# Kernel tuning notes

Measured on AMD Instinct MI355X. Metric: run time of the kernel, lower is better.

The kernel has to match this reference:

```python
import jax, jax.numpy as jnp
import numpy as np
import math

HEADS = 16
HIDDEN = 2048
D_K = HIDDEN // HEADS
BATCH = 2
SEQ = 2048
ROPE_THETA = 10000.0


def make_freqs_cis(seq_len, d_k, theta=ROPE_THETA):
    # Llama rotary frequencies; returned as (seq, d_k//2, 2) = (cos, sin)
    inv_freq = 1.0 / (theta ** (np.arange(0, d_k, 2, dtype=np.float32) / d_k))
    t = np.arange(seq_len, dtype=np.float32)
    ang = np.outer(t, inv_freq)  # (seq, d_k//2)
    return jnp.asarray(np.stack([np.cos(ang), np.sin(ang)], axis=-1))


def setup_inputs() -> dict:
    key = jax.random.key(0)
    ks = jax.random.split(key, 5)
    scale = 1.0 / math.sqrt(HIDDEN)
    return {
        "x": jax.random.normal(ks[0], (BATCH, SEQ, HIDDEN), dtype=jnp.float32),
        "freqs_cis": make_freqs_cis(SEQ, D_K),
        "wq": jax.random.normal(ks[1], (HIDDEN, HIDDEN), dtype=jnp.float32) * scale,
        "wk": jax.random.normal(ks[2], (HIDDEN, HIDDEN), dtype=jnp.float32) * scale,
        "wv": jax.random.normal(ks[3], (HIDDEN, HIDDEN), dtype=jnp.float32) * scale,
        "wo": jax.random.normal(ks[4], (HIDDEN, HIDDEN), dtype=jnp.float32) * scale,
    }


def _apply_rope(t, cos, sin):
    # t: (B, S, h, d_k); cos/sin: (1, S, 1, d_k//2)
    B, S, h, dk = t.shape
    tp = t.reshape(B, S, h, dk // 2, 2)
    t0, t1 = tp[..., 0], tp[..., 1]
    r0 = t0 * cos - t1 * sin
    r1 = t0 * sin + t1 * cos
    return jnp.stack([r0, r1], axis=-1).reshape(B, S, h, dk)


def reference(x, freqs_cis, wq, wk, wv, wo):
    B, S, H = x.shape
    h, dk = HEADS, H // HEADS
    # nn.Linear(bias=False): y = x @ W.T
    q = (x @ wq.T).reshape(B, S, h, dk)
    k = (x @ wk.T).reshape(B, S, h, dk)
    v = (x @ wv.T).reshape(B, S, h, dk)
    cos = freqs_cis[None, :, None, :, 0]
    sin = freqs_cis[None, :, None, :, 1]
    q = _apply_rope(q, cos, sin)
    k = _apply_rope(k, cos, sin)
    # (B, h, S, dk)
    q = q.transpose(0, 2, 1, 3)
    k = k.transpose(0, 2, 1, 3)
    v = v.transpose(0, 2, 1, 3)
    scores = jnp.einsum("bhqd,bhkd->bhqk", q, k) / math.sqrt(dk)
    causal = jnp.tril(jnp.ones((S, S), dtype=bool))
    scores = jnp.where(causal[None, None], scores, -jnp.inf)
    attn = jax.nn.softmax(scores, axis=-1)
    out = jnp.einsum("bhqk,bhkd->bhqd", attn, v)
    out = out.transpose(0, 2, 1, 3).reshape(B, S, H)
    return out @ wo.T
```

## Files before the change

kernel.cpp:

```cpp
#include <hip/hip_runtime.h>

#define SEQ 2048
#define HID 2048
#define NH 16
#define DK 128
#define NTOK 4096

typedef __bf16 bf16x8 __attribute__((ext_vector_type(8)));
typedef float f32x4 __attribute__((ext_vector_type(4)));
typedef unsigned int u32x4 __attribute__((ext_vector_type(4)));

__device__ __forceinline__ unsigned short f2bf(float f) {
  unsigned int u = __builtin_bit_cast(unsigned int, f);
  u += 0x7fffu + ((u >> 16) & 1u);
  return (unsigned short)(u >> 16);
}
__device__ __forceinline__ float bf2f(unsigned int lo16) {
  return __builtin_bit_cast(float, lo16 << 16);
}

__device__ __forceinline__ void async_cp16(const void* g, void* l) {
  __builtin_amdgcn_global_load_lds(
      (__attribute__((address_space(1))) void*)const_cast<void*>(g),
      (__attribute__((address_space(3))) void*)l, 16, 0, 0);
}

__global__ void convert_all_kernel(const float* __restrict__ x,
                                   const float* __restrict__ wq,
                                   const float* __restrict__ wk,
                                   const float* __restrict__ wv,
                                   const float* __restrict__ wo,
                                   const float* __restrict__ fc,
                                   unsigned short* __restrict__ xb,
                                   unsigned short* __restrict__ wqb,
                                   unsigned short* __restrict__ wkb,
                                   unsigned short* __restrict__ wvb,
                                   unsigned short* __restrict__ wob,
                                   unsigned int* __restrict__ fcb) {
  const int bid = blockIdx.x;
  if (bid >= 24576) {
    const int idx = (bid - 24576) * 256 + threadIdx.x;
    const int s = idx >> 6, d = idx & 63;
    const float2 cs = *(const float2*)(fc + s * 128 + 2 * d);
    fcb[idx] = (unsigned int)f2bf(cs.x) | ((unsigned int)f2bf(cs.y) << 16);
    return;
  }
  const float* src;
  unsigned short* dst;
  int base;
  if (bid < 8192) {
    src = x; dst = xb; base = bid;
  } else {
    const int t = (bid - 8192) >> 12;
    base = (bid - 8192) & 4095;
    src = (t == 0) ? wq : (t == 1) ? wk : (t == 2) ? wv : wo;
    dst = (t == 0) ? wqb : (t == 1) ? wkb : (t == 2) ? wvb : wob;
  }
  const int i = base * 256 + threadIdx.x;
  float4 v = ((const float4*)src)[i];
  ushort4 o;
  o.x = f2bf(v.x); o.y = f2bf(v.y); o.z = f2bf(v.z); o.w = f2bf(v.w);
  ((ushort4*)dst)[i] = o;
}

template<bool F32OUT>
__global__ __launch_bounds__(256, 2)
void gemm_bt_kernel(const unsigned short* __restrict__ A,
                    const unsigned short* __restrict__ B0,
                    const unsigned short* __restrict__ B1,
                    const unsigned short* __restrict__ B2,
                    unsigned short* __restrict__ O0,
                    unsigned short* __restrict__ O1,
                    unsigned short* __restrict__ O2,
                    float* __restrict__ Of,
                    const unsigned int* __restrict__ fcb) {
  __shared__ alignas(16) unsigned short As[128 * 64];
  __shared__ alignas(16) unsigned short Bs[128 * 64];

  const int bx = blockIdx.x, by = blockIdx.y;
  const unsigned short* B;
  unsigned short* Ob = nullptr;
  int sel = 0, col0;
  if (F32OUT) {
    B = B0;
    col0 = bx * 128;
  } else {
    sel = bx >> 4;
    B = (sel == 0) ? B0 : (sel == 1) ? B1 : B2;
    Ob = (sel == 0) ? O0 : (sel == 1) ? O1 : O2;
    col0 = (bx & 15) * 128;
  }
  const int row0 = by * 128;

  const int tid = threadIdx.x;
  const int wave = tid >> 6, lane = tid & 63;
  const int quad = lane >> 4, r = lane & 15;
  const int wm = wave >> 1, wn = wave & 1;
  const int jbase = wave * 256 + lane;

  f32x4 acc[4][4] = {};

  for (int k0 = 0; k0 < HID; k0 += 64) {
    for (int t = 0; t < 4; ++t) {
      const int j = jbase + t * 64;
      const int m = j >> 3;
      const int gc = (j & 7) ^ (m & 7);
      async_cp16(A + (size_t)(row0 + m) * HID + k0 + gc * 8, As + j * 8);
      async_cp16(B + (size_t)(col0 + m) * HID + k0 + gc * 8, Bs + j * 8);
    }
    __syncthreads();
    for (int kk = 0; kk < 2; ++kk) {
      bf16x8 af[4], bfr[4];
      for (int mt = 0; mt < 4; ++mt) {
        const int m = wm * 64 + mt * 16 + r;
        const int slot = (kk * 4 + quad) ^ (m & 7);
        af[mt] = __builtin_bit_cast(bf16x8, *(const u32x4*)(As + m * 64 + slot * 8));
      }
      for (int nt = 0; nt < 4; ++nt) {
        const int n = wn * 64 + nt * 16 + r;
        const int slot = (kk * 4 + quad) ^ (n & 7);
        bfr[nt] = __builtin_bit_cast(bf16x8, *(const u32x4*)(Bs + n * 64 + slot * 8));
      }
      for (int mt = 0; mt < 4; ++mt)
        for (int nt = 0; nt < 4; ++nt)
          acc[mt][nt] = __builtin_amdgcn_mfma_f32_16x16x32_bf16(
              af[mt], bfr[nt], acc[mt][nt], 0, 0, 0);
    }
    __syncthreads();
  }

  if (!F32OUT && sel == 2) {
    for (int mt = 0; mt < 4; ++mt) {
      const int row = row0 + wm * 64 + mt * 16 + quad * 4;
      const int b = row >> 11, s = row & (SEQ - 1);
      for (int nt = 0; nt < 4; ++nt) {
        const int col = col0 + wn * 64 + nt * 16 + r;
        ushort4 pk;
        pk.x = f2bf(acc[mt][nt][0]);
        pk.y = f2bf(acc[mt][nt][1]);
        pk.z = f2bf(acc[mt][nt][2]);
        pk.w = f2bf(acc[mt][nt][3]);
        *(ushort4*)(Ob + ((size_t)(b * HID + col)) * SEQ + s) = pk;
      }
    }
    return;
  }

  if (!F32OUT) {
    const float qs = (sel == 0) ? 0.12751743f : 1.0f;
    for (int mt = 0; mt < 4; ++mt) {
      const int row = row0 + wm * 64 + mt * 16 + quad * 4;
      for (int nt = 0; nt < 4; ++nt) {
        const int col = col0 + wn * 64 + nt * 16 + r;
        const int d = (wn * 64 + nt * 16 + r) >> 1;
        for (int v = 0; v < 4; ++v) {
          const int s = (row + v) & (SEQ - 1);
          const unsigned int u = fcb[s * 64 + d];
          const float c = bf2f(u & 0xffffu), sn = bf2f(u >> 16);
          const float val = acc[mt][nt][v];
          const float par = __shfl_xor(val, 1, 64);
          const float res = (r & 1) ? (par * sn + val * c)
                                    : (val * c - par * sn);
          Ob[(size_t)(row + v) * HID + col] = f2bf(res * qs);
        }
      }
    }
    return;
  }

  for (int mt = 0; mt < 4; ++mt) {
    const int row = row0 + wm * 64 + mt * 16 + quad * 4;
    for (int nt = 0; nt < 4; ++nt) {
      const int col = col0 + wn * 64 + nt * 16 + r;
      for (int v = 0; v < 4; ++v)
        Of[(size_t)(row + v) * HID + col] = acc[mt][nt][v];
    }
  }
}

__global__ __launch_bounds__(256, 2)
void flash_attn_kernel(const unsigned short* __restrict__ Qb,
                       const unsigned short* __restrict__ Kb,
                       const unsigned short* __restrict__ VtG,
                       unsigned short* __restrict__ Ob) {
  __shared__ alignas(16) unsigned short KsA[64 * 128];
  __shared__ alignas(16) unsigned short KsB[64 * 128];
  __shared__ alignas(16) unsigned short VsA[128 * 64];
  __shared__ alignas(16) unsigned short VsB[128 * 64];
  __shared__ alignas(16) unsigned short Ps[4][16 * 64];

  const int bx = blockIdx.x, bh = blockIdx.y;
  const int tid = threadIdx.x, wave = tid >> 6, lane = tid & 63;
  const int quad = lane >> 4, r = lane & 15;
  const int tokbase = (bh >> 4) * SEQ;
  const int h = bh & 15;

  const u32x4 onesv = {0x3F803F80u, 0x3F803F80u, 0x3F803F80u, 0x3F803F80u};

  auto stage = [&](int kt, unsigned short* Ks, unsigned short* Vs) {
    for (int t = 0; t < 4; ++t) {
      const int j = t * 256 + tid;
      const int n = j >> 4, slot = j & 15;
      const int gc = (slot & 8) | ((slot & 7) ^ (n & 7));
      async_cp16(Kb + (size_t)(tokbase + kt * 64 + n) * HID + h * DK + gc * 8,
                 Ks + j * 8);
    }
    for (int t = 0; t < 4; ++t) {
      const int j = t * 256 + tid;
      const int d = j >> 3, slot = j & 7;
      const int gc = slot ^ (d & 7);
      async_cp16(VtG + ((size_t)(bh * DK + d)) * SEQ + kt * 64 + gc * 8,
                 Vs + j * 8);
    }
  };

  for (int phase = 0; phase < 2; ++phase) {
    const int qt = phase ? (31 - bx) : bx;
    const int q0 = qt * 64;

    u32x4 qf[4];
    {
      const unsigned short* qrow =
          Qb + (size_t)(tokbase + q0 + wave * 16 + r) * HID + h * DK;
      for (int kk = 0; kk < 4; ++kk)
        qf[kk] = *(const u32x4*)(qrow + kk * 32 + quad * 8);
    }

    f32x4 o[8] = {};
    float m_i[4], l_i[4];
    for (int v = 0; v < 4; ++v) { m_i[v] = -__builtin_inff(); l_i[v] = 0.f; }

    auto body = [&](const unsigned short* Ks, const unsigned short* Vs, int kt) {
      f32x4 s[4];
      for (int nt = 0; nt < 4; ++nt) {
        f32x4 a = {};
        const int n = nt * 16 + r;
        for (int kk = 0; kk < 4; ++kk) {
          const int c = kk * 4 + quad;
          const int slot = (c & 8) | ((c & 7) ^ (r & 7));
          u32x4 bkf = *(const u32x4*)(Ks + n * 128 + slot * 8);
          a = __builtin_amdgcn_mfma_f32_16x16x32_bf16(
              __builtin_bit_cast(bf16x8, qf[kk]),
              __builtin_bit_cast(bf16x8, bkf), a, 0, 0, 0);
        }
        s[nt] = a;
      }

      if (kt == qt) {
        const int qrow_g = q0 + wave * 16 + quad * 4;
        for (int nt = 0; nt < 4; ++nt) {
          const int col = kt * 64 + nt * 16 + r;
          for (int v = 0; v < 4; ++v)
            if (col > qrow_g + v) s[nt][v] = -__builtin_inff();
        }
      }

      float mx[4];
      for (int v = 0; v < 4; ++v)
        mx[v] = fmaxf(fmaxf(s[0][v], s[1][v]), fmaxf(s[2][v], s[3][v]));
      for (int off = 1; off < 16; off <<= 1)
        for (int v = 0; v < 4; ++v)
          mx[v] = fmaxf(mx[v], __shfl_xor(mx[v], off, 64));

      float alpha[4];
      for (int v = 0; v < 4; ++v) {
        const float mnew = fmaxf(m_i[v], mx[v]);
        alpha[v] = exp2f(m_i[v] - mnew);
        m_i[v] = mnew;
      }

      unsigned short* ps = &Ps[wave][0];
      for (int nt = 0; nt < 4; ++nt) {
        const int chunk = nt * 2 + (r >> 3);
        for (int v = 0; v < 4; ++v) {
          const float p = exp2f(s[nt][v] - m_i[v]);
          const int row = quad * 4 + v;
          const int slot = chunk ^ (row & 7);
          ps[row * 64 + slot * 8 + (r & 7)] = f2bf(p);
        }
      }
      for (int dt = 0; dt < 8; ++dt)
        for (int v = 0; v < 4; ++v)
          o[dt][v] *= alpha[v];
      __asm__ volatile("" ::: "memory");

      f32x4 rsacc = {};
      for (int kk2 = 0; kk2 < 2; ++kk2) {
        const int c = kk2 * 4 + quad;
        const int aslot = c ^ (r & 7);
        u32x4 pa = *(const u32x4*)(ps + r * 64 + aslot * 8);
        rsacc = __builtin_amdgcn_mfma_f32_16x16x32_bf16(
            __builtin_bit_cast(bf16x8, pa),
            __builtin_bit_cast(bf16x8, onesv), rsacc, 0, 0, 0);
        for (int dt = 0; dt < 8; ++dt) {
          const int d = dt * 16 + r;
          const int bslot = c ^ (d & 7);
          u32x4 bv = *(const u32x4*)(Vs + d * 64 + bslot * 8);
          o[dt] = __builtin_amdgcn_mfma_f32_16x16x32_bf16(
              __builtin_bit_cast(bf16x8, pa),
              __builtin_bit_cast(bf16x8, bv), o[dt], 0, 0, 0);
        }
      }
      for (int v = 0; v < 4; ++v)
        l_i[v] = l_i[v] * alpha[v] + rsacc[v];
    };

    stage(0, KsA, VsA);
    int kt = 0;
    while (true) {
      __syncthreads();
      if (kt + 1 <= qt) stage(kt + 1, KsB, VsB);
      body(KsA, VsA, kt);
      if (++kt > qt) break;
      __syncthreads();
      if (kt + 1 <= qt) stage(kt + 1, KsA, VsA);
      body(KsB, VsB, kt);
      if (++kt > qt) break;
    }

    float li[4];
    for (int v = 0; v < 4; ++v) li[v] = 1.f / l_i[v];
    for (int dt = 0; dt < 8; ++dt)
      for (int v = 0; v < 4; ++v) {
        const size_t row = (size_t)tokbase + q0 + wave * 16 + quad * 4 + v;
        Ob[row * HID + h * DK + dt * 16 + r] = f2bf(o[dt][v] * li[v]);
      }
    __syncthreads();
  }
}

extern "C" void kernel_launch(void* const* d_in, const int* in_sizes, int n_in,
                              void* d_out, int out_size, void* d_ws, size_t ws_size,
                              hipStream_t stream) {
  const float* x  = (const float*)d_in[0];
  const float* fc = (const float*)d_in[1];
  const float* wq = (const float*)d_in[2];
  const float* wk = (const float*)d_in[3];
  const float* wv = (const float*)d_in[4];
  const float* wo = (const float*)d_in[5];
  float* out = (float*)d_out;

  unsigned short* xb  = (unsigned short*)d_ws;
  unsigned short* wqb = xb  + (size_t)NTOK * HID;
  unsigned short* wkb = wqb + (size_t)HID * HID;
  unsigned short* wvb = wkb + (size_t)HID * HID;
  unsigned short* wob = wvb + (size_t)HID * HID;
  unsigned short* qb  = wob + (size_t)HID * HID;
  unsigned short* kb  = qb  + (size_t)NTOK * HID;
  unsigned short* vtb = kb  + (size_t)NTOK * HID;
  unsigned short* ab  = vtb + (size_t)NTOK * HID;
  unsigned int*   fcb = (unsigned int*)(ab + (size_t)NTOK * HID);

  convert_all_kernel<<<24576 + 512, 256, 0, stream>>>(
      x, wq, wk, wv, wo, fc, xb, wqb, wkb, wvb, wob, fcb);

  gemm_bt_kernel<false><<<dim3(48, 32), 256, 0, stream>>>(
      xb, wqb, wkb, wvb, qb, kb, vtb, nullptr, fcb);

  flash_attn_kernel<<<dim3(16, 32), 256, 0, stream>>>(qb, kb, vtb, ab);

  gemm_bt_kernel<true><<<dim3(16, 32), 256, 0, stream>>>(
      ab, wob, nullptr, nullptr, nullptr, nullptr, nullptr, out, fcb);
}
```

Before: 375.6 us.

## Rewrite flash attention with 32x32 MFMA, transposed scores and split-K waves

Reworks the attention inner loop to use 32x32x16 bf16 MFMA with a transposed S = K·Q^T layout, so each lane holds one query's scores in registers. Two waves split each 64-key tile and their partial outputs are merged through LDS at the end. The LDS round trip for P and the ones-vector MFMA for row sums are replaced by in-register bf16 packing with permlane32 swaps and a direct sum. It also adds a lazy rescale that skips the output correction while the running max grows by at most 8, plus s_setprio hints around the MFMA blocks. The cost is an extra LDS merge with barriers per query tile and more complex code.

New measurement: 372.0 us. About the same (-0.9%).

```diff
diff --git a/kernel.cpp b/kernel.cpp
--- a/kernel.cpp
+++ b/kernel.cpp
@@ -8,6 +8,7 @@
 
 typedef __bf16 bf16x8 __attribute__((ext_vector_type(8)));
 typedef float f32x4 __attribute__((ext_vector_type(4)));
+typedef float f32x16 __attribute__((ext_vector_type(16)));
 typedef unsigned int u32x4 __attribute__((ext_vector_type(4)));
 
 __device__ __forceinline__ unsigned short f2bf(float f) {
@@ -187,22 +188,20 @@
   __shared__ alignas(16) unsigned short KsB[64 * 128];
   __shared__ alignas(16) unsigned short VsA[128 * 64];
   __shared__ alignas(16) unsigned short VsB[128 * 64];
-  __shared__ alignas(16) unsigned short Ps[4][16 * 64];
 
   const int bx = blockIdx.x, bh = blockIdx.y;
   const int tid = threadIdx.x, wave = tid >> 6, lane = tid & 63;
-  const int quad = lane >> 4, r = lane & 15;
+  const int l31 = lane & 31, hl = lane >> 5;
+  const int qgrp = wave >> 1, ksub = wave & 1;
   const int tokbase = (bh >> 4) * SEQ;
-  const int h = bh & 15;
-
-  const u32x4 onesv = {0x3F803F80u, 0x3F803F80u, 0x3F803F80u, 0x3F803F80u};
+  const int hh = bh & 15;
 
   auto stage = [&](int kt, unsigned short* Ks, unsigned short* Vs) {
     for (int t = 0; t < 4; ++t) {
       const int j = t * 256 + tid;
       const int n = j >> 4, slot = j & 15;
-      const int gc = (slot & 8) | ((slot & 7) ^ (n & 7));
-      async_cp16(Kb + (size_t)(tokbase + kt * 64 + n) * HID + h * DK + gc * 8,
+      const int gc = slot ^ (n & 15);
+      async_cp16(Kb + (size_t)(tokbase + kt * 64 + n) * HID + hh * DK + gc * 8,
                  Ks + j * 8);
     }
     for (int t = 0; t < 4; ++t) {
@@ -217,92 +216,104 @@
   for (int phase = 0; phase < 2; ++phase) {
     const int qt = phase ? (31 - bx) : bx;
     const int q0 = qt * 64;
-
-    u32x4 qf[4];
+    const int qloc = qgrp * 32 + l31;
+
+    u32x4 qf[8];
     {
       const unsigned short* qrow =
-          Qb + (size_t)(tokbase + q0 + wave * 16 + r) * HID + h * DK;
-      for (int kk = 0; kk < 4; ++kk)
-        qf[kk] = *(const u32x4*)(qrow + kk * 32 + quad * 8);
-    }
-
-    f32x4 o[8] = {};
-    float m_i[4], l_i[4];
-    for (int v = 0; v < 4; ++v) { m_i[v] = -__builtin_inff(); l_i[v] = 0.f; }
-
-    auto body = [&](const unsigned short* Ks, const unsigned short* Vs, int kt) {
-      f32x4 s[4];
-      for (int nt = 0; nt < 4; ++nt) {
-        f32x4 a = {};
-        const int n = nt * 16 + r;
-        for (int kk = 0; kk < 4; ++kk) {
-          const int c = kk * 4 + quad;
-          const int slot = (c & 8) | ((c & 7) ^ (r & 7));
-          u32x4 bkf = *(const u32x4*)(Ks + n * 128 + slot * 8);
-          a = __builtin_amdgcn_mfma_f32_16x16x32_bf16(
-              __builtin_bit_cast(bf16x8, qf[kk]),
-              __builtin_bit_cast(bf16x8, bkf), a, 0, 0, 0);
+          Qb + (size_t)(tokbase + q0 + qloc) * HID + hh * DK;
+#pragma unroll
+      for (int ks = 0; ks < 8; ++ks)
+        qf[ks] = *(const u32x4*)(qrow + ks * 16 + hl * 8);
+    }
+
+    f32x16 o[4] = {};
+    float m_i = -__builtin_inff(), l_i = 0.f;
+
+    auto body = [&](const unsigned short* Ks, const unsigned short* Vs,
+                    int kt) {
+      f32x16 s = {};
+      const unsigned short* krow = Ks + (size_t)(ksub * 32 + l31) * 128;
+      __builtin_amdgcn_s_setprio(1);
+#pragma unroll
+      for (int ks = 0; ks < 8; ++ks) {
+        const int slot = (ks * 2 + hl) ^ (lane & 15);
+        const u32x4 kf = *(const u32x4*)(krow + slot * 8);
+        s = __builtin_amdgcn_mfma_f32_32x32x16_bf16(
+            __builtin_bit_cast(bf16x8, kf),
+            __builtin_bit_cast(bf16x8, qf[ks]), s, 0, 0, 0);
+      }
+      __builtin_amdgcn_s_setprio(0);
+
+      float sv[16];
+#pragma unroll
+      for (int r = 0; r < 16; ++r) sv[r] = s[r];
+      if (kt == qt) {
+#pragma unroll
+        for (int r = 0; r < 16; ++r) {
+          const int kloc = ksub * 32 + (r & 3) + 8 * (r >> 2) + 4 * hl;
+          if (kloc > qloc) sv[r] = -__builtin_inff();
         }
-        s[nt] = a;
-      }
-
-      if (kt == qt) {
-        const int qrow_g = q0 + wave * 16 + quad * 4;
-        for (int nt = 0; nt < 4; ++nt) {
-          const int col = kt * 64 + nt * 16 + r;
-          for (int v = 0; v < 4; ++v)
-            if (col > qrow_g + v) s[nt][v] = -__builtin_inff();
+      }
+
+      float mx = fmaxf(fmaxf(fmaxf(sv[0], sv[1]), fmaxf(sv[2], sv[3])),
+                       fmaxf(fmaxf(sv[4], sv[5]), fmaxf(sv[6], sv[7])));
+      mx = fmaxf(mx,
+                 fmaxf(fmaxf(fmaxf(sv[8], sv[9]), fmaxf(sv[10], sv[11])),
+                       fmaxf(fmaxf(sv[12], sv[13]), fmaxf(sv[14], sv[15]))));
+      mx = fmaxf(mx, __shfl_xor(mx, 32, 64));
+
+      if (!__all(mx <= m_i + 8.f)) {
+        const float mnew = fmaxf(m_i, mx);
+        const float al = exp2f(m_i - mnew);
+        m_i = mnew;
+        l_i *= al;
+#pragma unroll
+        for (int dt = 0; dt < 4; ++dt)
+#pragma unroll
+          for (int r = 0; r < 16; ++r) o[dt][r] *= al;
+      }
+
+      float p[16];
+      float rs = 0.f;
+#pragma unroll
+      for (int r = 0; r < 16; ++r) {
+        p[r] = exp2f(fmaxf(sv[r] - m_i, -128.f));
+        rs += p[r];
+      }
+      l_i += rs + __shfl_xor(rs, 32, 64);
+
+      u32x4 af[2];
+#pragma unroll
+      for (int kk = 0; kk < 2; ++kk) {
+        unsigned int a, b2, c2, d2;
+        asm("v_cvt_pk_bf16_f32 %0, %1, %2"
+            : "=v"(a) : "v"(p[8 * kk + 0]), "v"(p[8 * kk + 1]));
+        asm("v_cvt_pk_bf16_f32 %0, %1, %2"
+            : "=v"(b2) : "v"(p[8 * kk + 2]), "v"(p[8 * kk + 3]));
+        asm("v_cvt_pk_bf16_f32 %0, %1, %2"
+            : "=v"(c2) : "v"(p[8 * kk + 4]), "v"(p[8 * kk + 5]));
+        asm("v_cvt_pk_bf16_f32 %0, %1, %2"
+            : "=v"(d2) : "v"(p[8 * kk + 6]), "v"(p[8 * kk + 7]));
+        asm("v_permlane32_swap_b32 %0, %1" : "+v"(a), "+v"(c2));
+        asm("v_permlane32_swap_b32 %0, %1" : "+v"(b2), "+v"(d2));
+        u32x4 t = {a, b2, c2, d2};
+        af[kk] = t;
+      }
+
+      __builtin_amdgcn_s_setprio(1);
+#pragma unroll
+      for (int kk = 0; kk < 2; ++kk)
+#pragma unroll
+        for (int dt = 0; dt < 4; ++dt) {
+          const int d = dt * 32 + l31;
+          const int slot = (ksub * 4 + kk * 2 + hl) ^ (d & 7);
+          const u32x4 vv = *(const u32x4*)(Vs + (size_t)d * 64 + slot * 8);
+          o[dt] = __builtin_amdgcn_mfma_f32_32x32x16_bf16(
+              __builtin_bit_cast(bf16x8, af[kk]),
+              __builtin_bit_cast(bf16x8, vv), o[dt], 0, 0, 0);
         }
-      }
-
-      float mx[4];
-      for (int v = 0; v < 4; ++v)
-        mx[v] = fmaxf(fmaxf(s[0][v], s[1][v]), fmaxf(s[2][v], s[3][v]));
-      for (int off = 1; off < 16; off <<= 1)
-        for (int v = 0; v < 4; ++v)
-          mx[v] = fmaxf(mx[v], __shfl_xor(mx[v], off, 64));
-
-      float alpha[4];
-      for (int v = 0; v < 4; ++v) {
-        const float mnew = fmaxf(m_i[v], mx[v]);
-        alpha[v] = exp2f(m_i[v] - mnew);
-        m_i[v] = mnew;
-      }
-
-      unsigned short* ps = &Ps[wave][0];
-      for (int nt = 0; nt < 4; ++nt) {
-        const int chunk = nt * 2 + (r >> 3);
-        for (int v = 0; v < 4; ++v) {
-          const float p = exp2f(s[nt][v] - m_i[v]);
-          const int row = quad * 4 + v;
-          const int slot = chunk ^ (row & 7);
-          ps[row * 64 + slot * 8 + (r & 7)] = f2bf(p);
-        }
-      }
-      for (int dt = 0; dt < 8; ++dt)
-        for (int v = 0; v < 4; ++v)
-          o[dt][v] *= alpha[v];
-      __asm__ volatile("" ::: "memory");
-
-      f32x4 rsacc = {};
-      for (int kk2 = 0; kk2 < 2; ++kk2) {
-        const int c = kk2 * 4 + quad;
-        const int aslot = c ^ (r & 7);
-        u32x4 pa = *(const u32x4*)(ps + r * 64 + aslot * 8);
-        rsacc = __builtin_amdgcn_mfma_f32_16x16x32_bf16(
-            __builtin_bit_cast(bf16x8, pa),
-            __builtin_bit_cast(bf16x8, onesv), rsacc, 0, 0, 0);
-        for (int dt = 0; dt < 8; ++dt) {
-          const int d = dt * 16 + r;
-          const int bslot = c ^ (d & 7);
-          u32x4 bv = *(const u32x4*)(Vs + d * 64 + bslot * 8);
-          o[dt] = __builtin_amdgcn_mfma_f32_16x16x32_bf16(
-              __builtin_bit_cast(bf16x8, pa),
-              __builtin_bit_cast(bf16x8, bv), o[dt], 0, 0, 0);
-        }
-      }
-      for (int v = 0; v < 4; ++v)
-        l_i[v] = l_i[v] * alpha[v] + rsacc[v];
+      __builtin_amdgcn_s_setprio(0);
     };
 
     stage(0, KsA, VsA);
@@ -318,13 +329,50 @@
       if (++kt > qt) break;
     }
 
-    float li[4];
-    for (int v = 0; v < 4; ++v) li[v] = 1.f / l_i[v];
-    for (int dt = 0; dt < 8; ++dt)
-      for (int v = 0; v < 4; ++v) {
-        const size_t row = (size_t)tokbase + q0 + wave * 16 + quad * 4 + v;
-        Ob[row * HID + h * DK + dt * 16 + r] = f2bf(o[dt][v] * li[v]);
-      }
+    __syncthreads();
+    float* obuf = (float*)(qgrp == 0 ? (void*)KsA : (void*)VsA);
+    float* mlbuf = (float*)KsB;
+    if (ksub == 1) {
+#pragma unroll
+      for (int dt = 0; dt < 4; ++dt)
+#pragma unroll
+        for (int r = 0; r < 16; ++r) {
+          const int qr = (r & 3) + 8 * (r >> 2) + 4 * hl;
+          obuf[qr * 128 + dt * 32 + l31] = o[dt][r];
+        }
+    }
+    if (lane < 32) {
+      mlbuf[wave * 64 + lane] = m_i;
+      mlbuf[wave * 64 + 32 + lane] = l_i;
+    }
+    __syncthreads();
+    if (ksub == 0) {
+      float f0[16], f1[16];
+#pragma unroll
+      for (int r = 0; r < 16; ++r) {
+        const int qr = (r & 3) + 8 * (r >> 2) + 4 * hl;
+        const float m0 = mlbuf[wave * 64 + qr];
+        const float l0 = mlbuf[wave * 64 + 32 + qr];
+        const float m1 = mlbuf[(wave + 1) * 64 + qr];
+        const float l1 = mlbuf[(wave + 1) * 64 + 32 + qr];
+        const float mm = fmaxf(m0, m1);
+        const float a0 = exp2f(fmaxf(m0 - mm, -128.f));
+        const float a1 = exp2f(fmaxf(m1 - mm, -128.f));
+        const float li = 1.f / (l0 * a0 + l1 * a1);
+        f0[r] = a0 * li;
+        f1[r] = a1 * li;
+      }
+#pragma unroll
+      for (int dt = 0; dt < 4; ++dt)
+#pragma unroll
+        for (int r = 0; r < 16; ++r) {
+          const int qr = (r & 3) + 8 * (r >> 2) + 4 * hl;
+          const float om =
+              o[dt][r] * f0[r] + obuf[qr * 128 + dt * 32 + l31] * f1[r];
+          Ob[(size_t)(tokbase + q0 + qgrp * 32 + qr) * HID + hh * DK +
+             dt * 32 + l31] = f2bf(om);
+        }
+    }
     __syncthreads();
   }
 }
```
